# Kernel optimization log

Hardware: AMD Instinct MI355X
Metric: run time of the kernel (lower is better)

Reference implementation:

```python
import jax, jax.numpy as jnp
import numpy as np

PH, PW = 7, 7            # output_size
SCALE = 0.25             # spatial_scale
SR = 2                   # sampling_ratio (fixed, jit-static)
ALIGNED = True


def setup_inputs() -> dict:
    key = jax.random.key(0)
    k1, k2, k3, k4, k5 = jax.random.split(key, 5)
    B, C, H, W = 4, 256, 200, 200
    N = 512
    img = H / SCALE  # 800.0 image size
    x = jax.random.normal(k1, (B, C, H, W), dtype=jnp.float32)
    bidx = jax.random.randint(k2, (N,), 0, B).astype(jnp.float32)
    cxy = jax.random.uniform(k3, (N, 2), minval=0.0, maxval=img)
    wh = jax.random.uniform(k4, (N, 2), minval=32.0, maxval=256.0)
    x1y1 = jnp.clip(cxy - wh / 2, 0.0, img - 1.0)
    x2y2 = jnp.clip(cxy + wh / 2, 0.0, img - 1.0)
    rois = jnp.concatenate([bidx[:, None], x1y1[:, 0:1], x1y1[:, 1:2],
                            x2y2[:, 0:1], x2y2[:, 1:2]], axis=1).astype(jnp.float32)
    return {"input": x, "rois": rois}


def _axis_samples(start, bin_size, P, size):
    """Sample coords along one axis. start/bin_size: [N]. Returns per-sample
    low/high integer indices, interp weights, and validity mask, all [N, P*SR]."""
    ib = jnp.arange(P, dtype=jnp.float32)           # bin index
    isr = jnp.arange(SR, dtype=jnp.float32)         # sample within bin
    # coord[n, p, s] = start + p*bin + (s+0.5)*bin/SR
    coord = (start[:, None, None]
             + ib[None, :, None] * bin_size[:, None, None]
             + (isr[None, None, :] + 0.5) * bin_size[:, None, None] / SR)
    coord = coord.reshape(coord.shape[0], P * SR)
    valid = (coord >= -1.0) & (coord <= size)
    c = jnp.maximum(coord, 0.0)
    lo_raw = jnp.floor(c).astype(jnp.int32)
    at_edge = lo_raw >= size - 1
    lo = jnp.where(at_edge, size - 1, lo_raw)
    hi = jnp.where(at_edge, size - 1, lo_raw + 1)
    cv = jnp.where(at_edge, jnp.float32(size - 1), c)
    frac = cv - lo.astype(jnp.float32)              # weight toward hi
    return lo, hi, frac, valid


def reference(input, rois):
    B, C, H, W = input.shape
    N = rois.shape[0]
    b = rois[:, 0].astype(jnp.int32)
    off = 0.5 if ALIGNED else 0.0
    sx = rois[:, 1] * SCALE - off
    sy = rois[:, 2] * SCALE - off
    ex = rois[:, 3] * SCALE - off
    ey = rois[:, 4] * SCALE - off
    rw, rh = ex - sx, ey - sy
    if not ALIGNED:
        rw = jnp.maximum(rw, 1.0)
        rh = jnp.maximum(rh, 1.0)
    bin_w, bin_h = rw / PW, rh / PH

    yl, yh, fy, vy = _axis_samples(sy, bin_h, PH, H)   # [N, Sy]
    xl, xh, fx, vx = _axis_samples(sx, bin_w, PW, W)   # [N, Sx]

    featT = jnp.transpose(input, (0, 2, 3, 1))         # [B,H,W,C]

    def gather(yi, xi):  # -> [N, Sy, Sx, C]
        return featT[b[:, None, None], yi[:, :, None], xi[:, None, :]]

    hy, ly = (1.0 - fy), fy
    hx, lx = (1.0 - fx), fx
    w_ll = (hy[:, :, None] * hx[:, None, :])[..., None]
    w_lh = (hy[:, :, None] * lx[:, None, :])[..., None]
    w_hl = (ly[:, :, None] * hx[:, None, :])[..., None]
    w_hh = (ly[:, :, None] * lx[:, None, :])[..., None]

    val = (w_ll * gather(yl, xl) + w_lh * gather(yl, xh)
           + w_hl * gather(yh, xl) + w_hh * gather(yh, xh))
    mask = (vy[:, :, None] & vx[:, None, :])[..., None]
    val = jnp.where(mask, val, 0.0)                    # [N, Sy, Sx, C]

    # average pool the SRxSR samples per output bin
    val = val.reshape(N, PH, SR, PW, SR, C).mean(axis=(2, 4))  # [N,PH,PW,C]
    return jnp.transpose(val, (0, 3, 1, 2))            # [N,C,PH,PW]
```

## Files before the change

### kernel.cpp

```cpp
#include <hip/hip_runtime.h>


#define R_PH 7
#define R_PW 7
#define R_SR 2
#define R_SCALE 0.25f
#define R_B 4
#define R_C 256
#define R_H 200
#define R_W 200

__device__ __forceinline__ void axis_sample(float start, float bin, int p, int s, int size,
                                            int& lo, int& hi, float& wlo, float& whi) {
    float coord = (start + (float)p * bin) + ((float)s + 0.5f) * bin * (1.0f / R_SR);
    bool valid = (coord >= -1.0f) && (coord <= (float)size);
    float c = fmaxf(coord, 0.0f);
    int lo_raw = (int)floorf(c);
    bool at_edge = lo_raw >= size - 1;
    lo = at_edge ? size - 1 : lo_raw;
    hi = at_edge ? size - 1 : lo_raw + 1;
    float cv = at_edge ? (float)(size - 1) : c;
    float frac = cv - (float)lo;
    whi = valid ? frac : 0.0f;
    wlo = valid ? (1.0f - frac) : 0.0f;
}

__global__ void __launch_bounds__(256)
roi_align_fwd(const float* __restrict__ input,
              const float* __restrict__ rois,
              float* __restrict__ out, int total) {
    int idx = blockIdx.x * blockDim.x + threadIdx.x;
    if (idx >= total) return;

    int pw = idx % R_PW;
    int ph = (idx / R_PW) % R_PH;
    int c  = (idx / (R_PW * R_PH)) % R_C;
    int n  = idx / (R_PW * R_PH * R_C);

    const float* r = rois + (size_t)n * 5;
    int   b  = (int)r[0];
    float sx = r[1] * R_SCALE - 0.5f;
    float sy = r[2] * R_SCALE - 0.5f;
    float ex = r[3] * R_SCALE - 0.5f;
    float ey = r[4] * R_SCALE - 0.5f;
    float bin_w = (ex - sx) * (1.0f / R_PW);
    float bin_h = (ey - sy) * (1.0f / R_PH);

    const float* plane = input + (size_t)(b * R_C + c) * (R_H * R_W);

    int   ylo[R_SR], yhi[R_SR], xlo[R_SR], xhi[R_SR];
    float wylo[R_SR], wyhi[R_SR], wxlo[R_SR], wxhi[R_SR];
#pragma unroll
    for (int s = 0; s < R_SR; ++s) {
        axis_sample(sy, bin_h, ph, s, R_H, ylo[s], yhi[s], wylo[s], wyhi[s]);
        axis_sample(sx, bin_w, pw, s, R_W, xlo[s], xhi[s], wxlo[s], wxhi[s]);
    }

    float acc = 0.0f;
#pragma unroll
    for (int ys = 0; ys < R_SR; ++ys) {
        const float* row_lo = plane + ylo[ys] * R_W;
        const float* row_hi = plane + yhi[ys] * R_W;
#pragma unroll
        for (int xs = 0; xs < R_SR; ++xs) {
            float fll = row_lo[xlo[xs]];
            float flh = row_lo[xhi[xs]];
            float fhl = row_hi[xlo[xs]];
            float fhh = row_hi[xhi[xs]];
            acc += wylo[ys] * (wxlo[xs] * fll + wxhi[xs] * flh)
                 + wyhi[ys] * (wxlo[xs] * fhl + wxhi[xs] * fhh);
        }
    }
    out[idx] = acc * (1.0f / (R_SR * R_SR));
}

extern "C" void kernel_launch(void* const* d_in, const int* in_sizes, int n_in,
                              void* d_out, int out_size, void* d_ws, size_t ws_size,
                              hipStream_t stream) {
    const float* input = (const float*)d_in[0];
    const float* rois  = (const float*)d_in[1];
    float* out = (float*)d_out;
    int total = out_size;
    int block = 256;
    int grid = (total + block - 1) / block;
    roi_align_fwd<<<grid, block, 0, stream>>>(input, rois, out, total);
}
```

Measured before the change: 304.7 us.

## Transpose input to NHWC workspace and gather channel-contiguous per ROI block

Adds a tiled LDS transpose kernel that converts the NCHW feature map to NHWC in the workspace. A new ROI kernel assigns one block per ROI and channel half, loading float2 channel pairs coalesced across lanes. It stages results in LDS and writes the NCHW output contiguously. This trades a full-tensor transpose pass for coalesced bilinear gathers, and falls back to the old kernel if the workspace is too small.

Result: slower. 311.6 us (+2.3%).

```diff
diff --git a/kernel.cpp b/kernel.cpp
--- a/kernel.cpp
+++ b/kernel.cpp
@@ -9,6 +9,7 @@
 #define R_C 256
 #define R_H 200
 #define R_W 200
+#define R_HW (R_H * R_W)
 
 __device__ __forceinline__ void axis_sample(float start, float bin, int p, int s, int size,
                                             int& lo, int& hi, float& wlo, float& whi) {
@@ -23,6 +24,93 @@
     float frac = cv - (float)lo;
     whi = valid ? frac : 0.0f;
     wlo = valid ? (1.0f - frac) : 0.0f;
+}
+
+__global__ void __launch_bounds__(512)
+nchw_to_nhwc(const float* __restrict__ in, float* __restrict__ out) {
+    __shared__ float tile[64][65];
+    int p0 = blockIdx.x * 64;
+    int c0 = blockIdx.y * 64;
+    int b  = blockIdx.z;
+    int tx = threadIdx.x;
+    int ty = threadIdx.y;
+    const float* src = in + (size_t)b * R_C * R_HW;
+    float* dst = out + (size_t)b * R_HW * R_C;
+#pragma unroll
+    for (int i = 0; i < 64; i += 8)
+        tile[ty + i][tx] = src[(size_t)(c0 + ty + i) * R_HW + p0 + tx];
+    __syncthreads();
+#pragma unroll
+    for (int i = 0; i < 64; i += 8)
+        dst[(size_t)(p0 + ty + i) * R_C + c0 + tx] = tile[tx][ty + i];
+}
+
+#define LDS_STRIDE 130
+
+__global__ void __launch_bounds__(256)
+roi_align_nhwc(const float* __restrict__ feat,
+               const float* __restrict__ rois,
+               float* __restrict__ out) {
+    __shared__ float lds[49 * LDS_STRIDE];
+    int n     = blockIdx.x;
+    int chalf = blockIdx.y;
+    int t    = threadIdx.x;
+    int wave = t >> 6;
+    int lane = t & 63;
+    int cl   = lane * 2;
+    int c    = chalf * 128 + cl;
+
+    const float* r = rois + (size_t)n * 5;
+    int   b  = (int)r[0];
+    float sx = r[1] * R_SCALE - 0.5f;
+    float sy = r[2] * R_SCALE - 0.5f;
+    float ex = r[3] * R_SCALE - 0.5f;
+    float ey = r[4] * R_SCALE - 0.5f;
+    float bin_w = (ex - sx) * (1.0f / R_PW);
+    float bin_h = (ey - sy) * (1.0f / R_PH);
+
+    const float* base = feat + (size_t)b * R_HW * R_C + c;
+
+    for (int bin = wave; bin < R_PH * R_PW; bin += 4) {
+        int ph = bin / 7;
+        int pw = bin - ph * 7;
+
+        int   ylo[R_SR], yhi[R_SR], xlo[R_SR], xhi[R_SR];
+        float wyl[R_SR], wyh[R_SR], wxl[R_SR], wxh[R_SR];
+#pragma unroll
+        for (int s = 0; s < R_SR; ++s) {
+            axis_sample(sy, bin_h, ph, s, R_H, ylo[s], yhi[s], wyl[s], wyh[s]);
+            axis_sample(sx, bin_w, pw, s, R_W, xlo[s], xhi[s], wxl[s], wxh[s]);
+        }
+
+        float accx = 0.0f, accy = 0.0f;
+#pragma unroll
+        for (int ys = 0; ys < R_SR; ++ys) {
+#pragma unroll
+            for (int xs = 0; xs < R_SR; ++xs) {
+                const float2 fll = *(const float2*)(base + (size_t)(ylo[ys] * R_W + xlo[xs]) * R_C);
+                const float2 flh = *(const float2*)(base + (size_t)(ylo[ys] * R_W + xhi[xs]) * R_C);
+                const float2 fhl = *(const float2*)(base + (size_t)(yhi[ys] * R_W + xlo[xs]) * R_C);
+                const float2 fhh = *(const float2*)(base + (size_t)(yhi[ys] * R_W + xhi[xs]) * R_C);
+                accx += wyl[ys] * (wxl[xs] * fll.x + wxh[xs] * flh.x)
+                      + wyh[ys] * (wxl[xs] * fhl.x + wxh[xs] * fhh.x);
+                accy += wyl[ys] * (wxl[xs] * fll.y + wxh[xs] * flh.y)
+                      + wyh[ys] * (wxl[xs] * fhl.y + wxh[xs] * fhh.y);
+            }
+        }
+        float2 res;
+        res.x = accx * (1.0f / (R_SR * R_SR));
+        res.y = accy * (1.0f / (R_SR * R_SR));
+        *(float2*)&lds[bin * LDS_STRIDE + cl] = res;
+    }
+    __syncthreads();
+
+    float* outn = out + (size_t)n * (R_C * 49) + (size_t)chalf * (128 * 49);
+    for (int i = t; i < 128 * 49; i += 256) {
+        int ch  = i / 49;
+        int bin = i - ch * 49;
+        outn[i] = lds[bin * LDS_STRIDE + ch];
+    }
 }
 
 __global__ void __launch_bounds__(256)
@@ -46,7 +134,7 @@
     float bin_w = (ex - sx) * (1.0f / R_PW);
     float bin_h = (ey - sy) * (1.0f / R_PH);
 
-    const float* plane = input + (size_t)(b * R_C + c) * (R_H * R_W);
+    const float* plane = input + (size_t)(b * R_C + c) * R_HW;
 
     int   ylo[R_SR], yhi[R_SR], xlo[R_SR], xhi[R_SR];
     float wylo[R_SR], wyhi[R_SR], wxlo[R_SR], wxhi[R_SR];
@@ -63,12 +151,8 @@
         const float* row_hi = plane + yhi[ys] * R_W;
 #pragma unroll
         for (int xs = 0; xs < R_SR; ++xs) {
-            float fll = row_lo[xlo[xs]];
-            float flh = row_lo[xhi[xs]];
-            float fhl = row_hi[xlo[xs]];
-            float fhh = row_hi[xhi[xs]];
-            acc += wylo[ys] * (wxlo[xs] * fll + wxhi[xs] * flh)
-                 + wyhi[ys] * (wxlo[xs] * fhl + wxhi[xs] * fhh);
+            acc += wylo[ys] * (wxlo[xs] * row_lo[xlo[xs]] + wxhi[xs] * row_lo[xhi[xs]])
+                 + wyhi[ys] * (wxlo[xs] * row_hi[xlo[xs]] + wxhi[xs] * row_hi[xhi[xs]]);
         }
     }
     out[idx] = acc * (1.0f / (R_SR * R_SR));
@@ -80,8 +164,18 @@
     const float* input = (const float*)d_in[0];
     const float* rois  = (const float*)d_in[1];
     float* out = (float*)d_out;
-    int total = out_size;
-    int block = 256;
-    int grid = (total + block - 1) / block;
-    roi_align_fwd<<<grid, block, 0, stream>>>(input, rois, out, total);
+    int N = in_sizes[1] / 5;
+
+    const size_t ws_needed = (size_t)R_B * R_C * R_HW * sizeof(float);
+    if (ws_size >= ws_needed) {
+        float* nhwc = (float*)d_ws;
+        dim3 tgrid(R_HW / 64, R_C / 64, R_B);
+        dim3 tblock(64, 8);
+        nchw_to_nhwc<<<tgrid, tblock, 0, stream>>>(input, nhwc);
+        dim3 ggrid(N, 2);
+        roi_align_nhwc<<<ggrid, 256, 0, stream>>>(nhwc, rois, out);
+    } else {
+        int total = out_size;
+        roi_align_fwd<<<(total + 255) / 256, 256, 0, stream>>>(input, rois, out, total);
+    }
 }
```

## Stage feature-map row strips in shared memory and bucket ROI bins per strip

Applied to the files above, without the earlier changes.

Adds a one-block pre-pass that buckets every (roi, ph) pair by batch and row strip into workspace lists. A new kernel then processes one (channel, batch, strip) per block: it copies a strip of rows plus halo into LDS with float4 loads and serves all bilinear samples that fall in that strip from LDS. This replaces scattered global gathers with one coalesced streaming read of the input. It relies on the sample rows staying inside the 56-row stage (bins under about 6 rows tall at this scale), depends on workspace size, and the single-block list build is serial.

Result: faster. 260.1 us (-14.7%).

```diff
diff --git a/kernel.cpp b/kernel.cpp
--- a/kernel.cpp
+++ b/kernel.cpp
@@ -5,10 +5,13 @@
 #define R_PW 7
 #define R_SR 2
 #define R_SCALE 0.25f
-#define R_B 4
 #define R_C 256
 #define R_H 200
 #define R_W 200
+#define R_HW (R_H * R_W)
+#define STRIP 50
+#define NSTRIP 4
+#define STAGE_ROWS 56
 
 __device__ __forceinline__ void axis_sample(float start, float bin, int p, int s, int size,
                                             int& lo, int& hi, float& wlo, float& whi) {
@@ -25,18 +28,100 @@
     wlo = valid ? (1.0f - frac) : 0.0f;
 }
 
+__global__ void __launch_bounds__(512)
+build_lists(const float* __restrict__ rois, int N, int* __restrict__ ws) {
+    __shared__ int lcnt[NSTRIP * 4];
+    int t = threadIdx.x;
+    if (t < 16) lcnt[t] = 0;
+    __syncthreads();
+    int* lists = ws + 16;
+    for (int n = t; n < N; n += 512) {
+        const float* r = rois + (size_t)n * 5;
+        int b = (int)r[0];
+        float sy = r[2] * R_SCALE - 0.5f;
+        float ey = r[4] * R_SCALE - 0.5f;
+        float binh = (ey - sy) * (1.0f / R_PH);
+        for (int ph = 0; ph < R_PH; ++ph) {
+            int lo, hi; float wl, wh;
+            axis_sample(sy, binh, ph, 0, R_H, lo, hi, wl, wh);
+            int bs = b * NSTRIP + lo / STRIP;
+            int pos = atomicAdd(&lcnt[bs], 1);
+            lists[bs * (N * R_PH) + pos] = (n << 3) | ph;
+        }
+    }
+    __syncthreads();
+    if (t < 16) ws[t] = lcnt[t];
+}
+
+__global__ void __launch_bounds__(512)
+roi_strip(const float* __restrict__ input,
+          const float* __restrict__ rois,
+          const int* __restrict__ ws, int N,
+          float* __restrict__ out) {
+    __shared__ float pl[STAGE_ROWS * R_W];
+    int c = blockIdx.x;
+    int b = blockIdx.y;
+    int s = blockIdx.z;
+    int r0 = s * STRIP;
+    int nrows = min(STAGE_ROWS, R_H - r0);
+
+    const float4* src = (const float4*)(input + (size_t)(b * R_C + c) * R_HW + r0 * R_W);
+    float4* dstv = (float4*)pl;
+    int nf4 = nrows * (R_W / 4);
+    for (int i = threadIdx.x; i < nf4; i += 512) dstv[i] = src[i];
+
+    int m = ws[b * NSTRIP + s];
+    const int* list = ws + 16 + (b * NSTRIP + s) * (N * R_PH);
+    __syncthreads();
+
+    int total = m * R_PW;
+    for (int i = threadIdx.x; i < total; i += 512) {
+        int e  = i / R_PW;
+        int pw = i - e * R_PW;
+        int code = list[e];
+        int n  = code >> 3;
+        int ph = code & 7;
+        const float* r = rois + (size_t)n * 5;
+        float sx = r[1] * R_SCALE - 0.5f;
+        float sy = r[2] * R_SCALE - 0.5f;
+        float ex = r[3] * R_SCALE - 0.5f;
+        float ey = r[4] * R_SCALE - 0.5f;
+        float binw = (ex - sx) * (1.0f / R_PW);
+        float binh = (ey - sy) * (1.0f / R_PH);
+
+        int   ylo[R_SR], yhi[R_SR], xlo[R_SR], xhi[R_SR];
+        float wyl[R_SR], wyh[R_SR], wxl[R_SR], wxh[R_SR];
+#pragma unroll
+        for (int q = 0; q < R_SR; ++q) {
+            axis_sample(sy, binh, ph, q, R_H, ylo[q], yhi[q], wyl[q], wyh[q]);
+            axis_sample(sx, binw, pw, q, R_W, xlo[q], xhi[q], wxl[q], wxh[q]);
+        }
+
+        float acc = 0.0f;
+#pragma unroll
+        for (int ys = 0; ys < R_SR; ++ys) {
+            const float* rlo = pl + (ylo[ys] - r0) * R_W;
+            const float* rhi = pl + (yhi[ys] - r0) * R_W;
+#pragma unroll
+            for (int xs = 0; xs < R_SR; ++xs) {
+                acc += wyl[ys] * (wxl[xs] * rlo[xlo[xs]] + wxh[xs] * rlo[xhi[xs]])
+                     + wyh[ys] * (wxl[xs] * rhi[xlo[xs]] + wxh[xs] * rhi[xhi[xs]]);
+            }
+        }
+        out[(size_t)(n * R_C + c) * 49 + ph * R_PW + pw] = acc * 0.25f;
+    }
+}
+
 __global__ void __launch_bounds__(256)
 roi_align_fwd(const float* __restrict__ input,
               const float* __restrict__ rois,
               float* __restrict__ out, int total) {
     int idx = blockIdx.x * blockDim.x + threadIdx.x;
     if (idx >= total) return;
-
     int pw = idx % R_PW;
     int ph = (idx / R_PW) % R_PH;
     int c  = (idx / (R_PW * R_PH)) % R_C;
     int n  = idx / (R_PW * R_PH * R_C);
-
     const float* r = rois + (size_t)n * 5;
     int   b  = (int)r[0];
     float sx = r[1] * R_SCALE - 0.5f;
@@ -45,9 +130,7 @@
     float ey = r[4] * R_SCALE - 0.5f;
     float bin_w = (ex - sx) * (1.0f / R_PW);
     float bin_h = (ey - sy) * (1.0f / R_PH);
-
-    const float* plane = input + (size_t)(b * R_C + c) * (R_H * R_W);
-
+    const float* plane = input + (size_t)(b * R_C + c) * R_HW;
     int   ylo[R_SR], yhi[R_SR], xlo[R_SR], xhi[R_SR];
     float wylo[R_SR], wyhi[R_SR], wxlo[R_SR], wxhi[R_SR];
 #pragma unroll
@@ -55,7 +138,6 @@
         axis_sample(sy, bin_h, ph, s, R_H, ylo[s], yhi[s], wylo[s], wyhi[s]);
         axis_sample(sx, bin_w, pw, s, R_W, xlo[s], xhi[s], wxlo[s], wxhi[s]);
     }
-
     float acc = 0.0f;
 #pragma unroll
     for (int ys = 0; ys < R_SR; ++ys) {
@@ -63,12 +145,8 @@
         const float* row_hi = plane + yhi[ys] * R_W;
 #pragma unroll
         for (int xs = 0; xs < R_SR; ++xs) {
-            float fll = row_lo[xlo[xs]];
-            float flh = row_lo[xhi[xs]];
-            float fhl = row_hi[xlo[xs]];
-            float fhh = row_hi[xhi[xs]];
-            acc += wylo[ys] * (wxlo[xs] * fll + wxhi[xs] * flh)
-                 + wyhi[ys] * (wxlo[xs] * fhl + wxhi[xs] * fhh);
+            acc += wylo[ys] * (wxlo[xs] * row_lo[xlo[xs]] + wxhi[xs] * row_lo[xhi[xs]])
+                 + wyhi[ys] * (wxlo[xs] * row_hi[xlo[xs]] + wxhi[xs] * row_hi[xhi[xs]]);
         }
     }
     out[idx] = acc * (1.0f / (R_SR * R_SR));
@@ -80,8 +158,16 @@
     const float* input = (const float*)d_in[0];
     const float* rois  = (const float*)d_in[1];
     float* out = (float*)d_out;
-    int total = out_size;
-    int block = 256;
-    int grid = (total + block - 1) / block;
-    roi_align_fwd<<<grid, block, 0, stream>>>(input, rois, out, total);
+    int N = in_sizes[1] / 5;
+
+    size_t ws_needed = (size_t)(16 + 16 * N * R_PH) * sizeof(int);
+    if (ws_size >= ws_needed) {
+        int* ws = (int*)d_ws;
+        build_lists<<<1, 512, 0, stream>>>(rois, N, ws);
+        dim3 grid(R_C, 4, NSTRIP);
+        roi_strip<<<grid, 512, 0, stream>>>(input, rois, ws, N, out);
+    } else {
+        int total = out_size;
+        roi_align_fwd<<<(total + 255) / 256, 256, 0, stream>>>(input, rois, out, total);
+    }
 }
```

## Stage whole feature planes in LDS and precompute per-ROI sample metadata

Applied to the files above, without the earlier changes.

Adds a metadata kernel that buckets ROIs by batch index and precomputes packed sample indices and half-precision interpolation weights per bin row and column. The main kernel then gives each (channel, batch) pair one block, which copies the full 200x200 plane into shared memory and computes every output for ROIs in that batch from LDS. This replaces scattered global gathers with one coalesced plane read per block. In exchange it uses 160 KB of LDS per block, which limits occupancy. Storing weights in fp16 loses precision, and the atomic-based ROI ordering is nondeterministic but does not change results.

Result: faster. 268.9 us (-11.8%).

```diff
diff --git a/kernel.cpp b/kernel.cpp
--- a/kernel.cpp
+++ b/kernel.cpp
@@ -1,14 +1,16 @@
 #include <hip/hip_runtime.h>
+#include <hip/hip_fp16.h>
 
 
 #define R_PH 7
 #define R_PW 7
 #define R_SR 2
 #define R_SCALE 0.25f
-#define R_B 4
 #define R_C 256
 #define R_H 200
 #define R_W 200
+#define R_HW (R_H * R_W)
+#define R_B 4
 
 __device__ __forceinline__ void axis_sample(float start, float bin, int p, int s, int size,
                                             int& lo, int& hi, float& wlo, float& whi) {
@@ -25,18 +27,114 @@
     wlo = valid ? (1.0f - frac) : 0.0f;
 }
 
+__device__ __forceinline__ unsigned pack_h2(float a, float b) {
+    __half2 h = __floats2half2_rn(a, b);
+    return *(unsigned*)&h;
+}
+
+__global__ void __launch_bounds__(512)
+build_meta(const float* __restrict__ rois, int N, int* __restrict__ ws) {
+    __shared__ int lc[R_B];
+    int t = threadIdx.x;
+    if (t < R_B) lc[t] = 0;
+    __syncthreads();
+    int*   blist = ws + R_B;
+    uint4* ymeta = (uint4*)(blist + R_B * N);
+    uint4* xmeta = ymeta + N * R_PH;
+
+    for (int n = t; n < N; n += 512) {
+        const float* r = rois + (size_t)n * 5;
+        int b = (int)r[0];
+        int pos = atomicAdd(&lc[b], 1);
+        blist[b * N + pos] = n;
+        float sx = r[1] * R_SCALE - 0.5f;
+        float sy = r[2] * R_SCALE - 0.5f;
+        float ex = r[3] * R_SCALE - 0.5f;
+        float ey = r[4] * R_SCALE - 0.5f;
+        float binw = (ex - sx) * (1.0f / R_PW);
+        float binh = (ey - sy) * (1.0f / R_PH);
+        for (int p = 0; p < R_PH; ++p) {
+            int lo0, hi0, lo1, hi1; float wl0, wh0, wl1, wh1;
+            axis_sample(sy, binh, p, 0, R_H, lo0, hi0, wl0, wh0);
+            axis_sample(sy, binh, p, 1, R_H, lo1, hi1, wl1, wh1);
+            uint4 m;
+            m.x = (unsigned)lo0 | ((unsigned)hi0 << 8) | ((unsigned)lo1 << 16) | ((unsigned)hi1 << 24);
+            m.y = pack_h2(wl0 * 0.25f, wh0 * 0.25f);
+            m.z = pack_h2(wl1 * 0.25f, wh1 * 0.25f);
+            m.w = 0;
+            ymeta[n * R_PH + p] = m;
+            axis_sample(sx, binw, p, 0, R_W, lo0, hi0, wl0, wh0);
+            axis_sample(sx, binw, p, 1, R_W, lo1, hi1, wl1, wh1);
+            m.x = (unsigned)lo0 | ((unsigned)hi0 << 8) | ((unsigned)lo1 << 16) | ((unsigned)hi1 << 24);
+            m.y = pack_h2(wl0, wh0);
+            m.z = pack_h2(wl1, wh1);
+            m.w = 0;
+            xmeta[n * R_PH + p] = m;
+        }
+    }
+    __syncthreads();
+    if (t < R_B) ws[t] = lc[t];
+}
+
+__global__ void __launch_bounds__(1024, 4)
+roi_plane(const float* __restrict__ input,
+          const int* __restrict__ ws, int N,
+          float* __restrict__ out) {
+    __shared__ float pl[R_HW];
+    int c = blockIdx.x;
+    int b = blockIdx.y;
+    int t = threadIdx.x;
+
+    const float4* src = (const float4*)(input + (size_t)(b * R_C + c) * R_HW);
+    float4* dst = (float4*)pl;
+    for (int i = t; i < R_HW / 4; i += 1024) dst[i] = src[i];
+
+    int cnt = ws[b];
+    const int*   blist = ws + R_B + b * N;
+    const uint4* ymeta = (const uint4*)(ws + R_B + R_B * N);
+    const uint4* xmeta = ymeta + N * R_PH;
+    __syncthreads();
+
+    int items = cnt * 49;
+    for (int i = t; i < items; i += 1024) {
+        int e  = i / 49;
+        int rr = i - e * 49;
+        int ph = rr / 7;
+        int pw = rr - ph * 7;
+        int n  = blist[e];
+        uint4 ym = ymeta[n * R_PH + ph];
+        uint4 xm = xmeta[n * R_PH + pw];
+
+        const float* p0 = pl + (ym.x & 255u) * R_W;
+        const float* p1 = pl + ((ym.x >> 8) & 255u) * R_W;
+        const float* p2 = pl + ((ym.x >> 16) & 255u) * R_W;
+        const float* p3 = pl + (ym.x >> 24) * R_W;
+        int c0 = xm.x & 255u, c1 = (xm.x >> 8) & 255u, c2 = (xm.x >> 16) & 255u, c3 = xm.x >> 24;
+
+        float2 wy01 = __half22float2(*(const __half2*)&ym.y);
+        float2 wy23 = __half22float2(*(const __half2*)&ym.z);
+        float2 wx01 = __half22float2(*(const __half2*)&xm.y);
+        float2 wx23 = __half22float2(*(const __half2*)&xm.z);
+
+        float s0 = wx01.x * p0[c0] + wx01.y * p0[c1] + wx23.x * p0[c2] + wx23.y * p0[c3];
+        float s1 = wx01.x * p1[c0] + wx01.y * p1[c1] + wx23.x * p1[c2] + wx23.y * p1[c3];
+        float s2 = wx01.x * p2[c0] + wx01.y * p2[c1] + wx23.x * p2[c2] + wx23.y * p2[c3];
+        float s3 = wx01.x * p3[c0] + wx01.y * p3[c1] + wx23.x * p3[c2] + wx23.y * p3[c3];
+        out[(size_t)(n * R_C + c) * 49 + rr] =
+            wy01.x * s0 + wy01.y * s1 + wy23.x * s2 + wy23.y * s3;
+    }
+}
+
 __global__ void __launch_bounds__(256)
 roi_align_fwd(const float* __restrict__ input,
               const float* __restrict__ rois,
               float* __restrict__ out, int total) {
     int idx = blockIdx.x * blockDim.x + threadIdx.x;
     if (idx >= total) return;
-
     int pw = idx % R_PW;
     int ph = (idx / R_PW) % R_PH;
     int c  = (idx / (R_PW * R_PH)) % R_C;
     int n  = idx / (R_PW * R_PH * R_C);
-
     const float* r = rois + (size_t)n * 5;
     int   b  = (int)r[0];
     float sx = r[1] * R_SCALE - 0.5f;
@@ -45,9 +143,7 @@
     float ey = r[4] * R_SCALE - 0.5f;
     float bin_w = (ex - sx) * (1.0f / R_PW);
     float bin_h = (ey - sy) * (1.0f / R_PH);
-
-    const float* plane = input + (size_t)(b * R_C + c) * (R_H * R_W);
-
+    const float* plane = input + (size_t)(b * R_C + c) * R_HW;
     int   ylo[R_SR], yhi[R_SR], xlo[R_SR], xhi[R_SR];
     float wylo[R_SR], wyhi[R_SR], wxlo[R_SR], wxhi[R_SR];
 #pragma unroll
@@ -55,7 +151,6 @@
         axis_sample(sy, bin_h, ph, s, R_H, ylo[s], yhi[s], wylo[s], wyhi[s]);
         axis_sample(sx, bin_w, pw, s, R_W, xlo[s], xhi[s], wxlo[s], wxhi[s]);
     }
-
     float acc = 0.0f;
 #pragma unroll
     for (int ys = 0; ys < R_SR; ++ys) {
@@ -63,12 +158,8 @@
         const float* row_hi = plane + yhi[ys] * R_W;
 #pragma unroll
         for (int xs = 0; xs < R_SR; ++xs) {
-            float fll = row_lo[xlo[xs]];
-            float flh = row_lo[xhi[xs]];
-            float fhl = row_hi[xlo[xs]];
-            float fhh = row_hi[xhi[xs]];
-            acc += wylo[ys] * (wxlo[xs] * fll + wxhi[xs] * flh)
-                 + wyhi[ys] * (wxlo[xs] * fhl + wxhi[xs] * fhh);
+            acc += wylo[ys] * (wxlo[xs] * row_lo[xlo[xs]] + wxhi[xs] * row_lo[xhi[xs]])
+                 + wyhi[ys] * (wxlo[xs] * row_hi[xlo[xs]] + wxhi[xs] * row_hi[xhi[xs]]);
         }
     }
     out[idx] = acc * (1.0f / (R_SR * R_SR));
@@ -80,8 +171,17 @@
     const float* input = (const float*)d_in[0];
     const float* rois  = (const float*)d_in[1];
     float* out = (float*)d_out;
-    int total = out_size;
-    int block = 256;
-    int grid = (total + block - 1) / block;
-    roi_align_fwd<<<grid, block, 0, stream>>>(input, rois, out, total);
+    int N = in_sizes[1] / 5;
+
+    size_t ws_needed = (size_t)(R_B + R_B * N) * sizeof(int)
+                     + (size_t)2 * N * R_PH * sizeof(uint4);
+    if (ws_size >= ws_needed) {
+        int* ws = (int*)d_ws;
+        build_meta<<<1, 512, 0, stream>>>(rois, N, ws);
+        dim3 grid(R_C, R_B);
+        roi_plane<<<grid, 1024, 0, stream>>>(input, ws, N, out);
+    } else {
+        int total = out_size;
+        roi_align_fwd<<<(total + 255) / 256, 256, 0, stream>>>(input, rois, out, total);
+    }
 }
```
